# Kernel tuning notes

Hardware: AMD Instinct MI355X
Metric: run time of the kernel (lower is better)

## Reference

```python
import jax, jax.numpy as jnp
import numpy as np

L = 8       # num_layers
D = 512     # embed_dim
H = 8       # num_heads
HD = D // H # head_dim = 64
V = 256     # vocab_size
T = 2048    # seq len (= context_length)
B = 4       # batch
FF = 4 * D  # mlp hidden
EPS = 1e-5


def setup_inputs() -> dict:
    key = jax.random.key(0)
    ks = jax.random.split(key, 18)
    g = lambda k, shape: (jax.random.normal(k, shape, jnp.float32) * 0.02)
    return {
        "x": jax.random.randint(ks[0], (B, T), 0, V),
        "tok_emb": g(ks[1], (V, D)),
        "pos_emb": g(ks[2], (T, D)),
        "attn_w": g(ks[3], (L, D, 3 * D)),
        "attn_b": g(ks[4], (L, 3 * D)),
        "proj_w": g(ks[5], (L, D, D)),
        "proj_b": g(ks[6], (L, D)),
        "ln1_g": jnp.ones((L, D), jnp.float32),
        "ln1_b": jnp.zeros((L, D), jnp.float32),
        "ln2_g": jnp.ones((L, D), jnp.float32),
        "ln2_b": jnp.zeros((L, D), jnp.float32),
        "ff1_w": g(ks[7], (L, D, FF)),
        "ff1_b": g(ks[8], (L, FF)),
        "ff2_w": g(ks[9], (L, FF, D)),
        "ff2_b": g(ks[10], (L, D)),
        "lnf_g": jnp.ones((D,), jnp.float32),
        "lnf_b": jnp.zeros((D,), jnp.float32),
    }


def _ln(x, g, b):
    m = jnp.mean(x, axis=-1, keepdims=True)
    v = jnp.mean(jnp.square(x - m), axis=-1, keepdims=True)
    return (x - m) * jax.lax.rsqrt(v + EPS) * g + b


def reference(x, tok_emb, pos_emb, attn_w, attn_b, proj_w, proj_b,
              ln1_g, ln1_b, ln2_g, ln2_b, ff1_w, ff1_b, ff2_w, ff2_b,
              lnf_g, lnf_b):
    Bx, Tx = x.shape
    h = tok_emb[x] + pos_emb[:Tx]                     # [B,T,D]
    causal = jnp.tril(jnp.ones((Tx, Tx), bool))       # [T,T]
    scale = 1.0 / np.sqrt(HD)
    for i in range(L):
        hn = _ln(h, ln1_g[i], ln1_b[i])
        qkv = hn @ attn_w[i] + attn_b[i]              # [B,T,3D]
        qkv = qkv.reshape(Bx, Tx, 3, H, HD)
        q = qkv[:, :, 0].transpose(0, 2, 1, 3)        # [B,H,T,HD]
        k = qkv[:, :, 1].transpose(0, 2, 1, 3)
        v = qkv[:, :, 2].transpose(0, 2, 1, 3)
        scores = jnp.einsum('bhqd,bhkd->bhqk', q, k) * scale
        scores = jnp.where(causal, scores, jnp.float32(-1e9))
        attn = jax.nn.softmax(scores, axis=-1)        # dropout identity at eval
        o = jnp.einsum('bhqk,bhkd->bhqd', attn, v)
        o = o.transpose(0, 2, 1, 3).reshape(Bx, Tx, D)
        h = h + o @ proj_w[i] + proj_b[i]
        hn2 = _ln(h, ln2_g[i], ln2_b[i])
        ff = jax.nn.gelu(hn2 @ ff1_w[i] + ff1_b[i], approximate=False)
        h = h + ff @ ff2_w[i] + ff2_b[i]
    logits = _ln(h, lnf_g, lnf_b) @ tok_emb.T         # tied lm_head
    return logits
```

## Files before the change

### kernel.cpp

```cpp
#include <hip/hip_runtime.h>

#define TT 2048
#define BB 4
#define DD 512
#define HH 8
#define LL 8
#define FFD 2048
#define VV 256
#define ROWS (BB*TT)

typedef short bf16x4 __attribute__((ext_vector_type(4)));
typedef short bf16x8 __attribute__((ext_vector_type(8)));
typedef float f32x4 __attribute__((ext_vector_type(4)));

#define GL2LDS(gp, lp) __builtin_amdgcn_global_load_lds( \
    (const __attribute__((address_space(1))) unsigned*)(gp), \
    (__attribute__((address_space(3))) unsigned*)(lp), 16, 0, 0)

__device__ __forceinline__ float bf2f(short s){
  union { unsigned u; float f; } x; x.u = ((unsigned)(unsigned short)s) << 16; return x.f;
}
__device__ __forceinline__ short f2bf(float f){
  union { float f; unsigned u; } x; x.f = f;
  unsigned r = (x.u + 0x7fffu + ((x.u >> 16) & 1u)) >> 16;
  return (short)(unsigned short)r;
}
__device__ __forceinline__ float ex2(float x){
  float r; asm("v_exp_f32 %0, %1" : "=v"(r) : "v"(x)); return r;
}
__device__ __forceinline__ unsigned cvtpk(float lo, float hi){
  unsigned r; asm("v_cvt_pk_bf16_f32 %0, %1, %2" : "=v"(r) : "v"(lo), "v"(hi)); return r;
}
__device__ __forceinline__ float xmax32(float x){ return fmaxf(x, __shfl_xor(x, 32)); }
__device__ __forceinline__ float xadd32(float x){ return x + __shfl_xor(x, 32); }

__device__ __forceinline__ float gelu_f(float v){
  float x = v * 0.70710678118f;
  float a = fabsf(x);
  float t = 1.0f / (1.0f + 0.3275911f * a);
  float poly = t*(0.254829592f + t*(-0.284496736f + t*(1.421413741f +
               t*(-1.453152027f + t*1.061405429f))));
  float er = 1.0f - poly * ex2(-1.44269504f * a * a);
  er = (x < 0.f) ? -er : er;
  return 0.5f * v * (1.0f + er);
}

__global__ __launch_bounds__(128) void embed_kernel(const int* __restrict__ x,
    const float* __restrict__ tok, const float* __restrict__ pos, float* __restrict__ h){
  int row = blockIdx.x;
  int t = row & (TT-1);
  int id = x[row];
  const float4 a = *(const float4*)&tok[(size_t)id*DD + threadIdx.x*4];
  const float4 p = *(const float4*)&pos[(size_t)t*DD + threadIdx.x*4];
  float4 r; r.x=a.x+p.x; r.y=a.y+p.y; r.z=a.z+p.z; r.w=a.w+p.w;
  *(float4*)&h[(size_t)row*DD + threadIdx.x*4] = r;
}

__global__ __launch_bounds__(256) void ln_kernel(const float* __restrict__ xx,
    const float* __restrict__ gw, const float* __restrict__ bw, short* __restrict__ out){
  const int lane = threadIdx.x & 63, w = threadIdx.x >> 6;
  const int row = blockIdx.x*4 + w;
  const float* xp = xx + (size_t)row*DD + lane*8;
  float4 a = *(const float4*)xp, c = *(const float4*)(xp+4);
  float xv[8] = {a.x,a.y,a.z,a.w,c.x,c.y,c.z,c.w};
  float s1 = 0.f, s2 = 0.f;
  #pragma unroll
  for (int e=0;e<8;e++){ s1 += xv[e]; s2 += xv[e]*xv[e]; }
  #pragma unroll
  for (int off=1; off<64; off<<=1){
    s1 += __shfl_xor(s1, off);
    s2 += __shfl_xor(s2, off);
  }
  const float m = s1 * (1.0f/DD);
  const float rstd = rsqrtf(s2*(1.0f/DD) - m*m + 1e-5f);
  const float4 g0 = *(const float4*)(gw + lane*8), g1 = *(const float4*)(gw + lane*8 + 4);
  const float4 b0 = *(const float4*)(bw + lane*8), b1 = *(const float4*)(bw + lane*8 + 4);
  float gg[8] = {g0.x,g0.y,g0.z,g0.w,g1.x,g1.y,g1.z,g1.w};
  float bb[8] = {b0.x,b0.y,b0.z,b0.w,b1.x,b1.y,b1.z,b1.w};
  short r[8];
  #pragma unroll
  for (int e=0;e<8;e++) r[e] = f2bf((xv[e]-m)*rstd*gg[e] + bb[e]);
  *(bf16x8*)&out[(size_t)row*DD + lane*8] = *(const bf16x8*)r;
}

__global__ __launch_bounds__(256) void transpose_cast_kernel(const float* __restrict__ src,
    short* __restrict__ dst, int R, int C){
  __shared__ float tile[32][33];
  size_t off = (size_t)blockIdx.z * R * C;
  src += off; dst += off;
  int c0 = blockIdx.x*32, r0 = blockIdx.y*32;
  int tx = threadIdx.x & 31, ty = threadIdx.x >> 5;
  #pragma unroll
  for (int i=0;i<4;i++) tile[ty + i*8][tx] = src[(size_t)(r0+ty+i*8)*C + c0 + tx];
  __syncthreads();
  #pragma unroll
  for (int i=0;i<4;i++) dst[(size_t)(c0+ty+i*8)*R + r0 + tx] = f2bf(tile[tx][ty+i*8]);
}

__global__ void cast_kernel(const float* __restrict__ in, short* __restrict__ out, int n){
  for (int i = blockIdx.x*blockDim.x + threadIdx.x; i < n; i += gridDim.x*blockDim.x)
    out[i] = f2bf(in[i]);
}

__device__ __forceinline__ void xcd_rowband(int gx, int gy, int& rowt, int& colt){
  int lin = blockIdx.y*gx + blockIdx.x;
  int x = lin & 7, j = lin >> 3;
  int jd = j / gy;
  rowt = x*(gx >> 3) + jd;
  colt = j - jd*gy;
}

template<int EPI>
__global__ __launch_bounds__(256) void gemm_dma(const short* __restrict__ A,
    const short* __restrict__ BT, const float* __restrict__ bias, void* __restrict__ C,
    int M, int N, int K)
{
  __shared__ short As[2][128*64];
  __shared__ short Bs[2][128*64];
  int rowt, colt;
  xcd_rowband(gridDim.x, gridDim.y, rowt, colt);
  const int row0 = rowt*128, col0 = colt*128;
  const int t = threadIdx.x, lane = t & 63, w = t >> 6;
  const int wm = w >> 1, wn = w & 1;
  const int rr = lane & 15, g = lane >> 4;
  f32x4 acc[4][4];
  #pragma unroll
  for (int m=0;m<4;m++)
    #pragma unroll
    for (int n=0;n<4;n++) acc[m][n] = (f32x4){0.f,0.f,0.f,0.f};

  const short* aP = A  + (size_t)(row0 + w*32 + (lane>>3))*K + (lane&7)*8;
  const short* bP = BT + (size_t)(col0 + w*32 + (lane>>3))*K + (lane&7)*8;

  const int nk = K >> 6;
  #pragma unroll
  for (int i=0;i<4;i++){
    GL2LDS(aP + (size_t)i*8*K, &As[0][w*2048 + i*512]);
    GL2LDS(bP + (size_t)i*8*K, &Bs[0][w*2048 + i*512]);
  }
  if (nk > 1){
    #pragma unroll
    for (int i=0;i<4;i++){
      GL2LDS(aP + (size_t)i*8*K + 64, &As[1][w*2048 + i*512]);
      GL2LDS(bP + (size_t)i*8*K + 64, &Bs[1][w*2048 + i*512]);
    }
  }
  for (int kt=0; kt<nk; kt++){
    if (kt < nk-1) asm volatile("s_waitcnt vmcnt(8)\n\ts_barrier" ::: "memory");
    else           asm volatile("s_waitcnt vmcnt(0)\n\ts_barrier" ::: "memory");
    const short* Ac = As[kt&1];
    const short* Bc = Bs[kt&1];
    #pragma unroll
    for (int ks=0; ks<2; ks++){
      bf16x8 af[4], bfr[4];
      #pragma unroll
      for (int m=0;m<4;m++) af[m]  = *(const bf16x8*)&Ac[(wm*64 + m*16 + rr)*64 + ks*32 + g*8];
      #pragma unroll
      for (int n=0;n<4;n++) bfr[n] = *(const bf16x8*)&Bc[(wn*64 + n*16 + rr)*64 + ks*32 + g*8];
      #pragma unroll
      for (int m=0;m<4;m++)
        #pragma unroll
        for (int n=0;n<4;n++)
          acc[m][n] = __builtin_amdgcn_mfma_f32_16x16x32_bf16(af[m], bfr[n], acc[m][n], 0,0,0);
    }
    if (kt+2 < nk){
      asm volatile("s_waitcnt lgkmcnt(0)\n\ts_barrier" ::: "memory");
      const int ko = (kt+2) << 6, nb = kt & 1;
      #pragma unroll
      for (int i=0;i<4;i++){
        GL2LDS(aP + (size_t)i*8*K + ko, &As[nb][w*2048 + i*512]);
        GL2LDS(bP + (size_t)i*8*K + ko, &Bs[nb][w*2048 + i*512]);
      }
    }
  }
  #pragma unroll
  for (int m=0;m<4;m++){
    #pragma unroll
    for (int n=0;n<4;n++){
      int cg = col0 + wn*64 + n*16 + rr;
      float bv = bias[cg];
      #pragma unroll
      for (int i=0;i<4;i++){
        int rg = row0 + wm*64 + m*16 + g*4 + i;
        float v = acc[m][n][i] + bv;
        size_t idx = (size_t)rg*N + cg;
        if constexpr (EPI==1) ((short*)C)[idx] = f2bf(v);
        else if constexpr (EPI==2) ((short*)C)[idx] = f2bf(gelu_f(v));
        else ((float*)C)[idx] += v;
      }
    }
  }
}

__global__ __launch_bounds__(256) void gemm_dma_n64(const short* __restrict__ A,
    const short* __restrict__ BT, const float* __restrict__ bias, float* __restrict__ C,
    int M, int N, int K)
{
  __shared__ short As[128*64];
  __shared__ short Bs[64*64];
  int rowt, colt;
  xcd_rowband(gridDim.x, gridDim.y, rowt, colt);
  const int row0 = rowt*128, col0 = colt*64;
  const int t = threadIdx.x, lane = t & 63, w = t >> 6;
  const int wm = w >> 1, wn = w & 1;
  const int rr = lane & 15, g = lane >> 4;
  f32x4 acc[4][2];
  #pragma unroll
  for (int m=0;m<4;m++)
    #pragma unroll
    for (int n=0;n<2;n++) acc[m][n] = (f32x4){0.f,0.f,0.f,0.f};

  const short* aP = A  + (size_t)(row0 + w*32 + (lane>>3))*K + (lane&7)*8;
  const short* bP = BT + (size_t)(col0 + w*16 + (lane>>3))*K + (lane&7)*8;
  short* aL = As + w*2048;
  short* bL = Bs + w*1024;

  for (int kt=0; kt<K; kt+=64){
    __syncthreads();
    #pragma unroll
    for (int i=0;i<4;i++) GL2LDS(aP + (size_t)i*8*K + kt, aL + i*512);
    #pragma unroll
    for (int i=0;i<2;i++) GL2LDS(bP + (size_t)i*8*K + kt, bL + i*512);
    __syncthreads();
    #pragma unroll
    for (int ks=0; ks<2; ks++){
      bf16x8 af[4], bfr[2];
      #pragma unroll
      for (int m=0;m<4;m++) af[m]  = *(const bf16x8*)&As[(wm*64 + m*16 + rr)*64 + ks*32 + g*8];
      #pragma unroll
      for (int n=0;n<2;n++) bfr[n] = *(const bf16x8*)&Bs[(wn*32 + n*16 + rr)*64 + ks*32 + g*8];
      #pragma unroll
      for (int m=0;m<4;m++)
        #pragma unroll
        for (int n=0;n<2;n++)
          acc[m][n] = __builtin_amdgcn_mfma_f32_16x16x32_bf16(af[m], bfr[n], acc[m][n], 0,0,0);
    }
  }
  #pragma unroll
  for (int m=0;m<4;m++){
    #pragma unroll
    for (int n=0;n<2;n++){
      int cg = col0 + wn*32 + n*16 + rr;
      float bv = bias[cg];
      #pragma unroll
      for (int i=0;i<4;i++){
        int rg = row0 + wm*64 + m*16 + g*4 + i;
        C[(size_t)rg*N + cg] += acc[m][n][i] + bv;
      }
    }
  }
}

template<int BM, int BN>
__global__ __launch_bounds__(256) void gemm_small(const short* __restrict__ A,
    const short* __restrict__ BT, float* __restrict__ C, int M, int N, int K)
{
  constexpr int FM = BM/32, FN = BN/32;
  __shared__ short As[BM][72];
  __shared__ short Bs[BN][72];
  const int row0 = blockIdx.x*BM, col0 = blockIdx.y*BN;
  const int t = threadIdx.x, lane = t & 63, w = t >> 6;
  const int wm = w >> 1, wn = w & 1;
  const int rr = lane & 15, kg = (lane >> 4)*8;
  f32x4 acc[FM][FN];
  #pragma unroll
  for (int m=0;m<FM;m++)
    #pragma unroll
    for (int n=0;n<FN;n++) acc[m][n] = (f32x4){0.f,0.f,0.f,0.f};

  for (int kt=0; kt<K; kt+=64){
    #pragma unroll
    for (int i=0;i<BM/32;i++){
      int cid = t + i*256; int r = cid >> 3; int c = (cid & 7)*8;
      *(bf16x8*)&As[r][c] = *(const bf16x8*)&A[(size_t)(row0+r)*K + kt + c];
    }
    #pragma unroll
    for (int i=0;i<BN/32;i++){
      int cid = t + i*256; int r = cid >> 3; int c = (cid & 7)*8;
      *(bf16x8*)&Bs[r][c] = *(const bf16x8*)&BT[(size_t)(col0+r)*K + kt + c];
    }
    __syncthreads();
    #pragma unroll
    for (int ks=0; ks<2; ks++){
      bf16x8 af[FM], bfr[FN];
      #pragma unroll
      for (int m=0;m<FM;m++) af[m] = *(const bf16x8*)&As[wm*FM*16 + m*16 + rr][ks*32 + kg];
      #pragma unroll
      for (int n=0;n<FN;n++) bfr[n] = *(const bf16x8*)&Bs[wn*FN*16 + n*16 + rr][ks*32 + kg];
      #pragma unroll
      for (int m=0;m<FM;m++)
        #pragma unroll
        for (int n=0;n<FN;n++)
          acc[m][n] = __builtin_amdgcn_mfma_f32_16x16x32_bf16(af[m], bfr[n], acc[m][n], 0,0,0);
    }
    __syncthreads();
  }
  #pragma unroll
  for (int m=0;m<FM;m++)
    #pragma unroll
    for (int n=0;n<FN;n++){
      int cg = col0 + wn*FN*16 + n*16 + rr;
      #pragma unroll
      for (int i=0;i<4;i++){
        int rg = row0 + wm*FM*16 + m*16 + (lane>>4)*4 + i;
        C[(size_t)rg*N + cg] = acc[m][n][i];
      }
    }
}

__device__ __forceinline__ void attn_tile(const short* __restrict__ Kc,
    const short* __restrict__ Vc, const bf16x8* qr, f32x4* oacc,
    float& mrun, float& lpart, int qi, int g, int qloc, bool diag)
{
  f32x4 sacc[4];
  #pragma unroll
  for (int f=0; f<4; f++) sacc[f] = (f32x4){0.f,0.f,0.f,0.f};
  __builtin_amdgcn_s_setprio(1);
  #pragma unroll
  for (int ks=0; ks<2; ks++){
    #pragma unroll
    for (int f=0; f<4; f++){
      bf16x8 kf = *(const bf16x8*)&Kc[(f*16 + qi)*64 + (((ks*4 + g) ^ (qi&7))*8)];
      sacc[f] = __builtin_amdgcn_mfma_f32_16x16x32_bf16(kf, qr[ks], sacc[f], 0,0,0);
    }
  }
  __builtin_amdgcn_s_setprio(0);

  float p[4][4];
  if (diag){
    #pragma unroll
    for (int f=0; f<4; f++)
      #pragma unroll
      for (int i=0; i<4; i++){
        int koffs = f*16 + g*4 + i;
        p[f][i] = (koffs <= qloc) ? sacc[f][i] : -1e30f;
      }
  } else {
    #pragma unroll
    for (int f=0; f<4; f++)
      #pragma unroll
      for (int i=0; i<4; i++) p[f][i] = sacc[f][i];
  }
  float t0 = fmaxf(fmaxf(p[0][0],p[0][1]), fmaxf(p[0][2],p[0][3]));
  float t1 = fmaxf(fmaxf(p[1][0],p[1][1]), fmaxf(p[1][2],p[1][3]));
  float t2 = fmaxf(fmaxf(p[2][0],p[2][1]), fmaxf(p[2][2],p[2][3]));
  float t3 = fmaxf(fmaxf(p[3][0],p[3][1]), fmaxf(p[3][2],p[3][3]));
  float tm = fmaxf(fmaxf(t0,t1), fmaxf(t2,t3));
  tm = fmaxf(tm, __shfl_xor(tm, 16));
  tm = xmax32(tm);
  if (!__all(tm <= mrun + 8.f)){
    float mnew = fmaxf(mrun, tm);
    float corr = ex2(mrun - mnew);
    lpart *= corr;
    #pragma unroll
    for (int mf=0; mf<4; mf++)
      #pragma unroll
      for (int i=0; i<4; i++) oacc[mf][i] *= corr;
    mrun = mnew;
  }
  float ts = 0.f;
  #pragma unroll
  for (int f=0; f<4; f++)
    #pragma unroll
    for (int i=0; i<4; i++){
      float e = ex2(p[f][i] - mrun);
      p[f][i] = e;
      ts += e;
    }
  lpart += ts;

  __builtin_amdgcn_s_setprio(1);
  #pragma unroll
  for (int w2=0; w2<2; w2++){
    union { unsigned u[4]; bf16x8 v; } bfr;
    bfr.u[0] = cvtpk(p[2*w2  ][0], p[2*w2  ][1]);
    bfr.u[1] = cvtpk(p[2*w2  ][2], p[2*w2  ][3]);
    bfr.u[2] = cvtpk(p[2*w2+1][0], p[2*w2+1][1]);
    bfr.u[3] = cvtpk(p[2*w2+1][2], p[2*w2+1][3]);
    #pragma unroll
    for (int mf=0; mf<4; mf++){
      const short* vp = &Vc[(mf*16 + qi)*72 + w2*32 + g*4];
      union { bf16x4 h[2]; bf16x8 v; } af;
      af.h[0] = *(const bf16x4*)vp;
      af.h[1] = *(const bf16x4*)(vp + 16);
      oacc[mf] = __builtin_amdgcn_mfma_f32_16x16x32_bf16(af.v, bfr.v, oacc[mf], 0,0,0);
    }
  }
  __builtin_amdgcn_s_setprio(0);
}

__global__ __launch_bounds__(256) void attn_kernel(const short* __restrict__ qkv, short* __restrict__ o){
  __shared__ __align__(16) char smem[34816];
  short* KsB = (short*)smem;
  short* VtB = (short*)(smem + 16384);
  float* Osh = (float*)smem;

  const int lin = blockIdx.x;
  const int xcd = lin & 7, idx = lin >> 3;
  const int bh = xcd*4 + (idx & 3);
  const int qp = idx >> 2;
  const int b = bh >> 3, hh = bh & 7;
  const int ql = qp, qh = 31 - qp;
  const int nt = qh + 1;

  const int t = threadIdx.x, lane = t & 63, wid = t >> 6;
  const int g = lane >> 4, qi = lane & 15;
  const int qloc = wid*16 + qi;
  const size_t base = (size_t)b*TT*3*DD + hh*64;

  bf16x8 qL[2], qH[2];
  {
    const float qs = 0.125f * 1.44269504f;
    const short* qpL = qkv + base + (size_t)(ql*64 + qloc)*3*DD + g*8;
    const short* qpH = qkv + base + (size_t)(qh*64 + qloc)*3*DD + g*8;
    qL[0] = *(const bf16x8*)&qpL[0]; qL[1] = *(const bf16x8*)&qpL[32];
    qH[0] = *(const bf16x8*)&qpH[0]; qH[1] = *(const bf16x8*)&qpH[32];
    #pragma unroll
    for (int j=0;j<8;j++){
      qL[0][j] = f2bf(qs * bf2f(qL[0][j]));
      qL[1][j] = f2bf(qs * bf2f(qL[1][j]));
      qH[0][j] = f2bf(qs * bf2f(qH[0][j]));
      qH[1][j] = f2bf(qs * bf2f(qH[1][j]));
    }
  }
  f32x4 oL[4], oH[4];
  #pragma unroll
  for (int mf=0; mf<4; mf++){ oL[mf] = (f32x4){0.f,0.f,0.f,0.f}; oH[mf] = (f32x4){0.f,0.f,0.f,0.f}; }
  float mL = -1e30f, lL = 0.f, mH = -1e30f, lH = 0.f;

  const short* ksrc = qkv + base + DD + (size_t)(wid*16 + (lane>>3))*3*DD
                      + (((lane&7) ^ (lane>>3))*8);
  const int vk = (t & 31)*2, vd = (t >> 5)*8;
  const short* vsrc = qkv + base + 2*DD + (size_t)vk*3*DD + vd;

  GL2LDS(ksrc, KsB + wid*1024);
  GL2LDS(ksrc + (size_t)8*3*DD, KsB + wid*1024 + 512);
  bf16x8 v0a = *(const bf16x8*)vsrc;
  bf16x8 v0b = *(const bf16x8*)(vsrc + 3*DD);
  bf16x8 vLoA = *(const bf16x8*)(vsrc + (size_t)64*3*DD);
  bf16x8 vLoB = *(const bf16x8*)(vsrc + (size_t)64*3*DD + 3*DD);
  asm volatile("s_waitcnt vmcnt(0)" ::: "memory");
  #pragma unroll
  for (int e=0;e<8;e++)
    *(unsigned*)&VtB[(vd+e)*72 + vk] =
        (unsigned)(unsigned short)v0a[e] | ((unsigned)(unsigned short)v0b[e] << 16);

  for (int kb = 0; kb < nt; kb++){
    asm volatile("s_waitcnt vmcnt(0) lgkmcnt(0)\n\ts_barrier" ::: "memory");
    bf16x8 vHiA = vLoA, vHiB = vLoB;
    if (kb+1 < nt){
      const size_t koff = (size_t)(kb+1)*64*3*DD;
      short* kd = KsB + ((kb+1)&1)*4096 + wid*1024;
      GL2LDS(ksrc + koff, kd);
      GL2LDS(ksrc + koff + (size_t)8*3*DD, kd + 512);
      short* Vn = VtB + ((kb+1)&1)*4608;
      #pragma unroll
      for (int e=0;e<8;e++)
        *(unsigned*)&Vn[(vd+e)*72 + vk] =
            (unsigned)(unsigned short)vLoA[e] | ((unsigned)(unsigned short)vLoB[e] << 16);
    }
    if (kb+2 < nt){
      const size_t koff2 = (size_t)(kb+2)*64*3*DD;
      vHiA = *(const bf16x8*)(vsrc + koff2);
      vHiB = *(const bf16x8*)(vsrc + koff2 + 3*DD);
    }
    const short* Kc = KsB + (kb&1)*4096;
    const short* Vc = VtB + (kb&1)*4608;

    attn_tile(Kc, Vc, qH, oH, mH, lH, qi, g, qloc, kb == nt-1);
    if (kb <= ql)
      attn_tile(Kc, Vc, qL, oL, mL, lL, qi, g, qloc, kb == ql);

    vLoA = vHiA; vLoB = vHiB;
  }

  lL += __shfl_xor(lL, 16); lL = xadd32(lL);
  lH += __shfl_xor(lH, 16); lH = xadd32(lH);

  const int orow = t >> 2, cc = (t & 3) * 16;
  #pragma unroll
  for (int s=0; s<2; s++){
    const f32x4* oacc = s ? oH : oL;
    const float inv = 1.f / (s ? lH : lL);
    const int q0 = (s ? qh : ql) * 64;
    __syncthreads();
    #pragma unroll
    for (int mf=0; mf<4; mf++)
      #pragma unroll
      for (int i=0; i<4; i++)
        Osh[qloc*65 + mf*16 + g*4 + i] = oacc[mf][i] * inv;
    __syncthreads();
    short tmp[16];
    #pragma unroll
    for (int e=0; e<16; e++) tmp[e] = f2bf(Osh[orow*65 + cc + e]);
    short* op = o + ((size_t)b*TT + q0 + orow)*DD + hh*64 + cc;
    *(bf16x8*)&op[0] = *(const bf16x8*)&tmp[0];
    *(bf16x8*)&op[8] = *(const bf16x8*)&tmp[8];
  }
}

extern "C" void kernel_launch(void* const* d_in, const int* in_sizes, int n_in,
                              void* d_out, int out_size, void* d_ws, size_t ws_size,
                              hipStream_t stream) {
  const int*   x      = (const int*)d_in[0];
  const float* tok    = (const float*)d_in[1];
  const float* pos    = (const float*)d_in[2];
  const float* attn_w = (const float*)d_in[3];
  const float* attn_b = (const float*)d_in[4];
  const float* proj_w = (const float*)d_in[5];
  const float* proj_b = (const float*)d_in[6];
  const float* ln1_g  = (const float*)d_in[7];
  const float* ln1_b  = (const float*)d_in[8];
  const float* ln2_g  = (const float*)d_in[9];
  const float* ln2_b  = (const float*)d_in[10];
  const float* ff1_w  = (const float*)d_in[11];
  const float* ff1_b  = (const float*)d_in[12];
  const float* ff2_w  = (const float*)d_in[13];
  const float* ff2_b  = (const float*)d_in[14];
  const float* lnf_g  = (const float*)d_in[15];
  const float* lnf_b  = (const float*)d_in[16];

  char* p = (char*)d_ws;
  float* h   = (float*)p; p += (size_t)ROWS*DD*4;
  short* hn  = (short*)p; p += (size_t)ROWS*DD*2;
  short* qkv = (short*)p; p += (size_t)ROWS*3*DD*2;
  short* ob  = (short*)p; p += (size_t)ROWS*DD*2;
  short* ffb = (short*)p; p += (size_t)ROWS*FFD*2;
  short* awT = (short*)p; p += (size_t)LL*3*DD*DD*2;
  short* pwT = (short*)p; p += (size_t)LL*DD*DD*2;
  short* f1T = (short*)p; p += (size_t)LL*FFD*DD*2;
  short* f2T = (short*)p; p += (size_t)LL*DD*FFD*2;
  short* lmT = (short*)p; p += (size_t)VV*DD*2;

  transpose_cast_kernel<<<dim3(48,16,8),256,0,stream>>>(attn_w, awT, DD, 3*DD);
  transpose_cast_kernel<<<dim3(16,16,8),256,0,stream>>>(proj_w, pwT, DD, DD);
  transpose_cast_kernel<<<dim3(64,16,8),256,0,stream>>>(ff1_w, f1T, DD, FFD);
  transpose_cast_kernel<<<dim3(16,64,8),256,0,stream>>>(ff2_w, f2T, FFD, DD);
  cast_kernel<<<128,256,0,stream>>>(tok, lmT, VV*DD);
  embed_kernel<<<ROWS,128,0,stream>>>(x, tok, pos, h);

  for (int l=0;l<LL;l++){
    ln_kernel<<<ROWS/4,256,0,stream>>>(h, ln1_g + l*DD, ln1_b + l*DD, hn);
    gemm_dma<1><<<dim3(ROWS/128, (3*DD)/128),256,0,stream>>>(
        hn, awT + (size_t)l*3*DD*DD, attn_b + (size_t)l*3*DD, qkv, ROWS, 3*DD, DD);
    attn_kernel<<<512,256,0,stream>>>(qkv, ob);
    gemm_dma_n64<<<dim3(ROWS/128, DD/64),256,0,stream>>>(
        ob, pwT + (size_t)l*DD*DD, proj_b + (size_t)l*DD, h, ROWS, DD, DD);
    ln_kernel<<<ROWS/4,256,0,stream>>>(h, ln2_g + l*DD, ln2_b + l*DD, hn);
    gemm_dma<2><<<dim3(ROWS/128, FFD/128),256,0,stream>>>(
        hn, f1T + (size_t)l*FFD*DD, ff1_b + (size_t)l*FFD, ffb, ROWS, FFD, DD);
    gemm_dma_n64<<<dim3(ROWS/128, DD/64),256,0,stream>>>(
        ffb, f2T + (size_t)l*DD*FFD, ff2_b + (size_t)l*DD, h, ROWS, DD, FFD);
  }
  ln_kernel<<<ROWS/4,256,0,stream>>>(h, lnf_g, lnf_b, hn);
  gemm_small<64,64><<<dim3(ROWS/64, VV/64),256,0,stream>>>(
      hn, lmT, (float*)d_out, ROWS, VV, DD);
}
```

Before: 1.557 ms.

## Restructure GEMM pipeline to triple-buffered BK=32 with single barrier per step

Changes the GEMM main loop from double-buffered 64-wide K tiles to triple-buffered 32-wide K tiles. The prefetch for step kt+2 is issued right after the barrier, before the MFMAs, which removes the second barrier per iteration. LDS use drops from 64KB to 48KB, which may allow more resident blocks. In exchange, each iteration does half the MFMA work per barrier, and the 32-element row stride in LDS may raise bank conflicts.

New measurement: 1.496 ms. 1.04x faster.

```diff
diff --git a/kernel.cpp b/kernel.cpp
--- a/kernel.cpp
+++ b/kernel.cpp
@@ -115,8 +115,8 @@
     const short* __restrict__ BT, const float* __restrict__ bias, void* __restrict__ C,
     int M, int N, int K)
 {
-  __shared__ short As[2][128*64];
-  __shared__ short Bs[2][128*64];
+  __shared__ short As[3][128*32];
+  __shared__ short Bs[3][128*32];
   int rowt, colt;
   xcd_rowband(gridDim.x, gridDim.y, rowt, colt);
   const int row0 = rowt*128, col0 = colt*128;
@@ -129,49 +129,49 @@
     #pragma unroll
     for (int n=0;n<4;n++) acc[m][n] = (f32x4){0.f,0.f,0.f,0.f};
 
-  const short* aP = A  + (size_t)(row0 + w*32 + (lane>>3))*K + (lane&7)*8;
-  const short* bP = BT + (size_t)(col0 + w*32 + (lane>>3))*K + (lane&7)*8;
-
-  const int nk = K >> 6;
-  #pragma unroll
-  for (int i=0;i<4;i++){
-    GL2LDS(aP + (size_t)i*8*K, &As[0][w*2048 + i*512]);
-    GL2LDS(bP + (size_t)i*8*K, &Bs[0][w*2048 + i*512]);
+  const int srow = lane >> 2;
+  const short* aP = A  + (size_t)(row0 + w*32 + srow)*K + (lane&3)*8;
+  const short* bP = BT + (size_t)(col0 + w*32 + srow)*K + (lane&3)*8;
+
+  const int nk = K >> 5;
+  #pragma unroll
+  for (int i=0;i<2;i++){
+    GL2LDS(aP + (size_t)i*16*K, &As[0][w*1024 + i*512]);
+    GL2LDS(bP + (size_t)i*16*K, &Bs[0][w*1024 + i*512]);
   }
   if (nk > 1){
     #pragma unroll
-    for (int i=0;i<4;i++){
-      GL2LDS(aP + (size_t)i*8*K + 64, &As[1][w*2048 + i*512]);
-      GL2LDS(bP + (size_t)i*8*K + 64, &Bs[1][w*2048 + i*512]);
-    }
-  }
+    for (int i=0;i<2;i++){
+      GL2LDS(aP + (size_t)i*16*K + 32, &As[1][w*1024 + i*512]);
+      GL2LDS(bP + (size_t)i*16*K + 32, &Bs[1][w*1024 + i*512]);
+    }
+  }
+  int cur = 0, st = 2;
   for (int kt=0; kt<nk; kt++){
-    if (kt < nk-1) asm volatile("s_waitcnt vmcnt(8)\n\ts_barrier" ::: "memory");
-    else           asm volatile("s_waitcnt vmcnt(0)\n\ts_barrier" ::: "memory");
-    const short* Ac = As[kt&1];
-    const short* Bc = Bs[kt&1];
-    #pragma unroll
-    for (int ks=0; ks<2; ks++){
-      bf16x8 af[4], bfr[4];
-      #pragma unroll
-      for (int m=0;m<4;m++) af[m]  = *(const bf16x8*)&Ac[(wm*64 + m*16 + rr)*64 + ks*32 + g*8];
-      #pragma unroll
-      for (int n=0;n<4;n++) bfr[n] = *(const bf16x8*)&Bc[(wn*64 + n*16 + rr)*64 + ks*32 + g*8];
-      #pragma unroll
-      for (int m=0;m<4;m++)
-        #pragma unroll
-        for (int n=0;n<4;n++)
-          acc[m][n] = __builtin_amdgcn_mfma_f32_16x16x32_bf16(af[m], bfr[n], acc[m][n], 0,0,0);
-    }
+    if (kt < nk-1) asm volatile("s_waitcnt vmcnt(4) lgkmcnt(0)\n\ts_barrier" ::: "memory");
+    else           asm volatile("s_waitcnt vmcnt(0) lgkmcnt(0)\n\ts_barrier" ::: "memory");
     if (kt+2 < nk){
-      asm volatile("s_waitcnt lgkmcnt(0)\n\ts_barrier" ::: "memory");
-      const int ko = (kt+2) << 6, nb = kt & 1;
-      #pragma unroll
-      for (int i=0;i<4;i++){
-        GL2LDS(aP + (size_t)i*8*K + ko, &As[nb][w*2048 + i*512]);
-        GL2LDS(bP + (size_t)i*8*K + ko, &Bs[nb][w*2048 + i*512]);
+      const int ko = (kt+2) << 5;
+      #pragma unroll
+      for (int i=0;i<2;i++){
+        GL2LDS(aP + (size_t)i*16*K + ko, &As[st][w*1024 + i*512]);
+        GL2LDS(bP + (size_t)i*16*K + ko, &Bs[st][w*1024 + i*512]);
       }
     }
+    const short* Ac = As[cur];
+    const short* Bc = Bs[cur];
+    bf16x8 af[4], bfr[4];
+    #pragma unroll
+    for (int m=0;m<4;m++) af[m]  = *(const bf16x8*)&Ac[(wm*64 + m*16 + rr)*32 + g*8];
+    #pragma unroll
+    for (int n=0;n<4;n++) bfr[n] = *(const bf16x8*)&Bc[(wn*64 + n*16 + rr)*32 + g*8];
+    #pragma unroll
+    for (int m=0;m<4;m++)
+      #pragma unroll
+      for (int n=0;n<4;n++)
+        acc[m][n] = __builtin_amdgcn_mfma_f32_16x16x32_bf16(af[m], bfr[n], acc[m][n], 0,0,0);
+    cur = (cur==2) ? 0 : cur+1;
+    st  = (st==2)  ? 0 : st+1;
   }
   #pragma unroll
   for (int m=0;m<4;m++){
```
